# Kernel optimization log

Hardware: AMD Instinct MI355X
Metric: run time of the kernel (lower is better)

The kernel has to match this reference:

```python
import jax, jax.numpy as jnp
import numpy as np

N_NODES = 100000
N_EDGES = 6400000
MIN_DIST = 5.0


def setup_inputs() -> dict:
    key = jax.random.key(0)
    k1, k2, k3 = jax.random.split(key, 3)
    pos = jax.random.normal(k1, (N_NODES, 2), dtype=jnp.float32)
    vel = jax.random.normal(k2, (N_NODES, 2), dtype=jnp.float32)
    edge_index = jax.random.randint(k3, (2, N_EDGES), 0, N_NODES, dtype=jnp.int64)
    return {"pos": pos, "vel": vel, "edge_index": edge_index}


def reference(pos, vel, edge_index):
    # h = [pos, vel] per node, shape [N, 4]
    h = jnp.concatenate([pos, vel], axis=-1)
    src, dst = edge_index[0], edge_index[1]  # PyG: h_j = h[src], h_i = h[dst]
    h_dif = h[src] - h[dst]                  # [E, 4]
    pos_dif = h_dif[:, :2]                   # [E, 2]
    vel_dif = h_dif[:, 2:]                   # [E, 2]

    norm = jnp.linalg.norm(pos_dif, axis=1)  # [E]
    safe_norm = jnp.where(norm > 0, norm, 1.0)
    # coll = -sigmoid(-10*(|d|-min_dist)) * d/|d|, nan_to_num(0) where |d|==0
    coll = jnp.where(
        (norm > 0)[:, None],
        -jax.nn.sigmoid(-10.0 * (norm - MIN_DIST))[:, None] * pos_dif / safe_norm[:, None],
        0.0,
    )                                        # [E, 2]
    mean_in = pos_dif / 30.0 + vel_dif       # [E, 2]

    n = pos.shape[0]
    add_out = jax.ops.segment_sum(coll, dst, num_segments=n)      # scatter add
    sums = jax.ops.segment_sum(mean_in, dst, num_segments=n)
    counts = jax.ops.segment_sum(jnp.ones((dst.shape[0], 1), pos.dtype), dst, num_segments=n)
    mean_out = sums / jnp.maximum(counts, 1.0)                    # scatter mean

    return add_out * 5.0 + mean_out          # [N, 2] acceleration
```

## Files before the change

kernel.cpp:

```cpp
#include <hip/hip_runtime.h>


#define DC      200
#define NBK     512
#define NSEG    512
#define EPB     12500
#define ORDCAP  14400
#define KB      13
#define KMAX    15
#define BLOCK   256
#define BBLOCK  1024
#define FBLOCK  1024

__device__ __forceinline__ void edge_math(float4 hs, float4 hd,
                                          float& cx, float& cy, float& mx, float& my) {
    float px = hs.x - hd.x;
    float py = hs.y - hd.y;
    float vx = hs.z - hd.z;
    float vy = hs.w - hd.w;
    float norm = sqrtf(px * px + py * py);
    cx = 0.0f; cy = 0.0f;
    if (norm > 0.0f) {
        float sig = 1.0f / (1.0f + expf(10.0f * (norm - 5.0f)));
        float scale = -sig / norm;
        cx = scale * px;
        cy = scale * py;
    }
    mx = px * (1.0f / 30.0f) + vx;
    my = py * (1.0f / 30.0f) + vy;
}

__global__ void prep_kernel(const float2* __restrict__ pos2,
                            const float2* __restrict__ vel2,
                            float4* __restrict__ h4, int n) {
    int i = blockIdx.x * blockDim.x + threadIdx.x;
    if (i < n) {
        float2 p = pos2[i];
        float2 v = vel2[i];
        h4[i] = make_float4(p.x, p.y, v.x, v.y);
    }
}

__global__ __launch_bounds__(BBLOCK) void bin_kernel(
        const int* __restrict__ ei, unsigned* __restrict__ binsout,
        int* __restrict__ inclT, int n_edges, int nbb) {
    __shared__ int hist[NBK];
    __shared__ int cur[NBK];
    __shared__ unsigned ord[EPB];
    __shared__ int wsum[16];
    __shared__ int wbase[16];

    const int tid  = threadIdx.x;
    const int lane = tid & 63;
    const int wv   = tid >> 6;
    const int bx   = blockIdx.x;
    const long long e0 = (long long)bx * EPB;
    const int n_my = (int)min((long long)EPB, (long long)n_edges - e0);
    if (n_my <= 0) return;

    const int* __restrict__ srow = ei + e0;
    const int* __restrict__ drow = ei + n_edges + e0;

    for (int i = tid; i < NBK; i += BBLOCK) hist[i] = 0;
    __syncthreads();

    int      bq[KB];
    unsigned wq[KB];
    #pragma unroll
    for (int q = 0; q < KB; ++q) {
        int idx = tid + q * BBLOCK;
        if (idx < n_my) {
            int d = drow[idx];
            int s = srow[idx];
            int b = (unsigned)d / DC;
            bq[q] = b;
            wq[q] = ((unsigned)s << 8) | (unsigned)(d - b * DC);
            atomicAdd(&hist[b], 1);
        } else {
            bq[q] = -1;
        }
    }
    __syncthreads();

    const int nw = NBK >> 6;
    int myinc = 0, myh = 0, myi = 0;
    if (wv < nw) {
        myi = (wv << 6) + lane;
        myh = hist[myi];
        int v = myh;
        #pragma unroll
        for (int m = 1; m < 64; m <<= 1) {
            int u = __shfl_up(v, m);
            if (lane >= m) v += u;
        }
        myinc = v;
        if (lane == 63) wsum[wv] = v;
    }
    __syncthreads();
    if (tid == 0) {
        int run = 0;
        for (int w = 0; w < nw; ++w) { wbase[w] = run; run += wsum[w]; }
    }
    __syncthreads();
    if (wv < nw) {
        int inc = myinc + wbase[wv];
        cur[myi] = inc - myh;
        inclT[(size_t)myi * nbb + bx] = inc;
    }
    __syncthreads();

    #pragma unroll
    for (int q = 0; q < KB; ++q) {
        if (bq[q] >= 0) {
            int p = atomicAdd(&cur[bq[q]], 1);
            ord[p] = wq[q];
        }
    }
    __syncthreads();

    unsigned* __restrict__ bo = binsout + e0;
    for (int i = tid; i < n_my; i += BBLOCK) bo[i] = ord[i];
}

__global__ __launch_bounds__(FBLOCK) void fused_kernel(
        const float4* __restrict__ h4, const unsigned* __restrict__ binsout,
        const int* __restrict__ inclT, float* __restrict__ out,
        int nbb, int n_nodes) {
    __shared__ unsigned ord2[ORDCAP];
    __shared__ unsigned sstart[NSEG];
    __shared__ int spfx[NSEG + 1];
    __shared__ int hist[DC];
    __shared__ int pfx[DC + 1];
    __shared__ int cur[DC];
    __shared__ int wsum[16];
    __shared__ int wbase[16];

    const int tid  = threadIdx.x;
    const int lane = tid & 63;
    const int wv   = tid >> 6;
    const int dc   = blockIdx.x;

    for (int j = tid; j < nbb; j += FBLOCK) {
        int hi = inclT[(size_t)dc * nbb + j];
        int lo = (dc > 0) ? inclT[(size_t)(dc - 1) * nbb + j] : 0;
        sstart[j] = (unsigned)j * EPB + (unsigned)lo;
        spfx[j + 1] = hi - lo;
    }
    for (int i = tid; i < DC; i += FBLOCK) hist[i] = 0;
    if (tid == 0) spfx[0] = 0;
    __syncthreads();

    const int nw = (nbb + 63) >> 6;
    int myv = 0, myj = -1;
    if (wv < nw) {
        myj = (wv << 6) + lane;
        int v = (myj < nbb) ? spfx[myj + 1] : 0;
        #pragma unroll
        for (int m = 1; m < 64; m <<= 1) {
            int u = __shfl_up(v, m);
            if (lane >= m) v += u;
        }
        myv = v;
        if (lane == 63) wsum[wv] = v;
    }
    __syncthreads();
    if (tid == 0) {
        int run = 0;
        for (int w = 0; w < nw; ++w) { wbase[w] = run; run += wsum[w]; }
    }
    __syncthreads();
    if (wv < nw && myj < nbb) spfx[myj + 1] = myv + wbase[wv];
    __syncthreads();
    int tot = spfx[nbb];
    if (tot > ORDCAP) tot = ORDCAP;
    for (int j = nbb + tid; j < NSEG; j += FBLOCK) spfx[j + 1] = tot;
    __syncthreads();

    unsigned wq[KMAX];
    #pragma unroll
    for (int q = 0; q < KMAX; ++q) {
        int p = tid + q * FBLOCK;
        if (p < tot) {
            int lo = 0;
            #pragma unroll
            for (int st = NSEG / 2; st >= 1; st >>= 1)
                if (spfx[lo + st] <= p) lo += st;
            unsigned w = binsout[sstart[lo] + (unsigned)(p - spfx[lo])];
            wq[q] = w;
            atomicAdd(&hist[w & 255u], 1);
        }
    }
    __syncthreads();

    const int nwh = (DC + 63) >> 6;
    int mvr = 0, mr = -1, mh = 0;
    if (wv < nwh) {
        mr = (wv << 6) + lane;
        mh = (mr < DC) ? hist[mr] : 0;
        int v = mh;
        #pragma unroll
        for (int m = 1; m < 64; m <<= 1) {
            int u = __shfl_up(v, m);
            if (lane >= m) v += u;
        }
        mvr = v;
        if (lane == 63) wsum[8 + wv] = v;
    }
    __syncthreads();
    if (tid == 0) {
        int run = 0;
        for (int w = 0; w < nwh; ++w) { wbase[8 + w] = run; run += wsum[8 + w]; }
    }
    __syncthreads();
    if (wv < nwh && mr < DC) {
        int inc = mvr + wbase[8 + wv];
        pfx[mr + 1] = inc;
        cur[mr] = inc - mh;
        if (mr == 0) pfx[0] = 0;
    }
    __syncthreads();

    #pragma unroll
    for (int q = 0; q < KMAX; ++q) {
        int p = tid + q * FBLOCK;
        if (p < tot) {
            int pp = atomicAdd(&cur[wq[q] & 255u], 1);
            ord2[pp] = wq[q] >> 8;
        }
    }
    __syncthreads();

    const int grp = tid >> 4;
    const int gl  = tid & 15;
    const int base = dc * DC;
    for (int r = grp; r < DC; r += FBLOCK / 16) {
        int n = base + r;
        if (n < n_nodes) {
            int st = pfx[r], en = pfx[r + 1];
            int cnt = en - st;
            float4 hd = h4[n];
            float a0 = 0.f, a1 = 0.f, a2 = 0.f, a3 = 0.f;
            for (int k = st + gl; k < en; k += 16) {
                unsigned s = ord2[k];
                float4 hs = h4[s];
                float cx, cy, mx, my;
                edge_math(hs, hd, cx, cy, mx, my);
                a0 += cx; a1 += cy; a2 += mx; a3 += my;
            }
            #pragma unroll
            for (int m = 8; m >= 1; m >>= 1) {
                a0 += __shfl_xor(a0, m);
                a1 += __shfl_xor(a1, m);
                a2 += __shfl_xor(a2, m);
                a3 += __shfl_xor(a3, m);
            }
            if (gl == 0) {
                float inv = 1.0f / fmaxf((float)cnt, 1.0f);
                float2 o;
                o.x = a0 * 5.0f + a2 * inv;
                o.y = a1 * 5.0f + a3 * inv;
                reinterpret_cast<float2*>(out)[n] = o;
            }
        }
    }
}

__global__ void edge_kernel(const float* __restrict__ pos,
                            const float* __restrict__ vel,
                            const int* __restrict__ ei,
                            float* __restrict__ acc,
                            int n_nodes, int n_edges) {
    int e = blockIdx.x * blockDim.x + threadIdx.x;
    if (e >= n_edges) return;
    int s = ei[e];
    int d = ei[n_edges + e];
    const float2* pos2 = reinterpret_cast<const float2*>(pos);
    const float2* vel2 = reinterpret_cast<const float2*>(vel);
    float4 hs = make_float4(pos2[s].x, pos2[s].y, vel2[s].x, vel2[s].y);
    float4 hd = make_float4(pos2[d].x, pos2[d].y, vel2[d].x, vel2[d].y);
    float cx, cy, mx, my;
    edge_math(hs, hd, cx, cy, mx, my);
    atomicAdd(&acc[0 * n_nodes + d], cx);
    atomicAdd(&acc[1 * n_nodes + d], cy);
    atomicAdd(&acc[2 * n_nodes + d], mx);
    atomicAdd(&acc[3 * n_nodes + d], my);
    atomicAdd(&acc[4 * n_nodes + d], 1.0f);
}

__global__ void finalize_kernel(const float* __restrict__ acc,
                                float* __restrict__ out, int n_nodes) {
    int i = blockIdx.x * blockDim.x + threadIdx.x;
    if (i >= n_nodes) return;
    float cx = acc[0 * n_nodes + i];
    float cy = acc[1 * n_nodes + i];
    float mx = acc[2 * n_nodes + i];
    float my = acc[3 * n_nodes + i];
    float cnt = acc[4 * n_nodes + i];
    float inv = 1.0f / fmaxf(cnt, 1.0f);
    float2 o;
    o.x = cx * 5.0f + mx * inv;
    o.y = cy * 5.0f + my * inv;
    reinterpret_cast<float2*>(out)[i] = o;
}

extern "C" void kernel_launch(void* const* d_in, const int* in_sizes, int n_in,
                              void* d_out, int out_size, void* d_ws, size_t ws_size,
                              hipStream_t stream) {
    const float* pos = (const float*)d_in[0];
    const float* vel = (const float*)d_in[1];
    const int*   ei  = (const int*)d_in[2];
    float* out = (float*)d_out;

    int n_nodes = in_sizes[0] / 2;
    int n_edges = in_sizes[2] / 2;

    int ndc = (n_nodes + DC - 1) / DC;
    int nbb = (int)(((long long)n_edges + EPB - 1) / EPB);

    size_t h_off    = 0;
    size_t bo_off   = (h_off + (size_t)n_nodes * 16 + 511) & ~(size_t)511;
    size_t incl_off = (bo_off + (size_t)nbb * EPB * 4 + 511) & ~(size_t)511;
    size_t need     = incl_off + (size_t)NBK * nbb * 4;

    if (ndc <= NBK && nbb <= NSEG && need <= ws_size &&
        (unsigned)n_nodes < (1u << 24)) {
        float4*   h4      = (float4*)((char*)d_ws + h_off);
        unsigned* binsout = (unsigned*)((char*)d_ws + bo_off);
        int*      inclT   = (int*)((char*)d_ws + incl_off);

        int grid_p = (n_nodes + BLOCK - 1) / BLOCK;
        prep_kernel<<<grid_p, BLOCK, 0, stream>>>(
            (const float2*)pos, (const float2*)vel, h4, n_nodes);

        bin_kernel<<<nbb, BBLOCK, 0, stream>>>(ei, binsout, inclT,
                                               n_edges, nbb);

        fused_kernel<<<ndc, FBLOCK, 0, stream>>>(h4, binsout, inclT, out,
                                                 nbb, n_nodes);
    } else {
        float* acc = (float*)d_ws;
        hipMemsetAsync(d_ws, 0, (size_t)5 * n_nodes * sizeof(float), stream);
        int grid_e = (n_edges + BLOCK - 1) / BLOCK;
        edge_kernel<<<grid_e, BLOCK, 0, stream>>>(pos, vel, ei, acc, n_nodes, n_edges);
        int grid_n = (n_nodes + BLOCK - 1) / BLOCK;
        finalize_kernel<<<grid_n, BLOCK, 0, stream>>>(acc, out, n_nodes);
    }
}
```

Baseline: 145.0 us.

## Fuse node packing into bin kernel, vectorize edge IO, replace segment search with map

Removes the separate prep kernel by having each bin_kernel block pack a slice of pos/vel into the float4 node buffer, saving one launch. The bin kernel now loads edge indices and stores binned output as int4 vectors when the block is full and aligned, keeping a scalar fallback for other cases. In the fused kernel, the per-element binary search over segment prefixes is replaced by a ushort lookup map built in shared memory (aliased onto ord2) plus a per-segment offset. This adds a serial per-thread fill loop for the map and more registers for the 16-entry edge queues.

```diff
diff --git a/kernel.cpp b/kernel.cpp
--- a/kernel.cpp
+++ b/kernel.cpp
@@ -7,6 +7,7 @@
 #define EPB     12500
 #define ORDCAP  14400
 #define KB      13
+#define KBV     16
 #define KMAX    15
 #define BLOCK   256
 #define BBLOCK  1024
@@ -30,23 +31,15 @@
     my = py * (1.0f / 30.0f) + vy;
 }
 
-__global__ void prep_kernel(const float2* __restrict__ pos2,
-                            const float2* __restrict__ vel2,
-                            float4* __restrict__ h4, int n) {
-    int i = blockIdx.x * blockDim.x + threadIdx.x;
-    if (i < n) {
-        float2 p = pos2[i];
-        float2 v = vel2[i];
-        h4[i] = make_float4(p.x, p.y, v.x, v.y);
-    }
-}
-
 __global__ __launch_bounds__(BBLOCK) void bin_kernel(
-        const int* __restrict__ ei, unsigned* __restrict__ binsout,
-        int* __restrict__ inclT, int n_edges, int nbb) {
+        const int* __restrict__ ei,
+        const float2* __restrict__ pos2, const float2* __restrict__ vel2,
+        float4* __restrict__ h4, unsigned* __restrict__ binsout,
+        int* __restrict__ inclT, int n_edges, int nbb,
+        int n_nodes, int hpb) {
+    __shared__ __align__(16) unsigned ord[EPB];
     __shared__ int hist[NBK];
     __shared__ int cur[NBK];
-    __shared__ unsigned ord[EPB];
     __shared__ int wsum[16];
     __shared__ int wbase[16];
 
@@ -58,28 +51,65 @@
     const int n_my = (int)min((long long)EPB, (long long)n_edges - e0);
     if (n_my <= 0) return;
 
+    {
+        int i0 = bx * hpb;
+        int i1 = min(n_nodes, i0 + hpb);
+        for (int i = i0 + tid; i < i1; i += BBLOCK) {
+            float2 p = pos2[i];
+            float2 v = vel2[i];
+            h4[i] = make_float4(p.x, p.y, v.x, v.y);
+        }
+    }
+
     const int* __restrict__ srow = ei + e0;
     const int* __restrict__ drow = ei + n_edges + e0;
 
     for (int i = tid; i < NBK; i += BBLOCK) hist[i] = 0;
     __syncthreads();
 
-    int      bq[KB];
-    unsigned wq[KB];
-    #pragma unroll
-    for (int q = 0; q < KB; ++q) {
-        int idx = tid + q * BBLOCK;
-        if (idx < n_my) {
-            int d = drow[idx];
-            int s = srow[idx];
-            int b = (unsigned)d / DC;
-            bq[q] = b;
-            wq[q] = ((unsigned)s << 8) | (unsigned)(d - b * DC);
-            atomicAdd(&hist[b], 1);
-        } else {
-            bq[q] = -1;
-        }
-    }
+    const bool vec = (n_my == EPB) && ((n_edges & 3) == 0) && ((EPB & 3) == 0);
+    const int nvec = EPB >> 2;
+
+    int      bq[KBV];
+    unsigned wq[KBV];
+    #pragma unroll
+    for (int q = 0; q < KBV; ++q) bq[q] = -1;
+
+    if (vec) {
+        const int4* __restrict__ s4 = reinterpret_cast<const int4*>(srow);
+        const int4* __restrict__ d4 = reinterpret_cast<const int4*>(drow);
+        #pragma unroll
+        for (int q = 0; q < 4; ++q) {
+            int v = tid + q * BBLOCK;
+            if (v < nvec) {
+                int4 ss = s4[v];
+                int4 dd = d4[v];
+                #pragma unroll
+                for (int j = 0; j < 4; ++j) {
+                    int d = (&dd.x)[j];
+                    int s = (&ss.x)[j];
+                    int b = (int)((unsigned)d / DC);
+                    bq[q * 4 + j] = b;
+                    wq[q * 4 + j] = ((unsigned)s << 8) | (unsigned)(d - b * DC);
+                }
+            }
+        }
+    } else {
+        #pragma unroll
+        for (int q = 0; q < KB; ++q) {
+            int idx = tid + q * BBLOCK;
+            if (idx < n_my) {
+                int d = drow[idx];
+                int s = srow[idx];
+                int b = (int)((unsigned)d / DC);
+                bq[q] = b;
+                wq[q] = ((unsigned)s << 8) | (unsigned)(d - b * DC);
+            }
+        }
+    }
+    #pragma unroll
+    for (int q = 0; q < KBV; ++q)
+        if (bq[q] >= 0) atomicAdd(&hist[bq[q]], 1);
     __syncthreads();
 
     const int nw = NBK >> 6;
@@ -110,7 +140,7 @@
     __syncthreads();
 
     #pragma unroll
-    for (int q = 0; q < KB; ++q) {
+    for (int q = 0; q < KBV; ++q) {
         if (bq[q] >= 0) {
             int p = atomicAdd(&cur[bq[q]], 1);
             ord[p] = wq[q];
@@ -118,8 +148,14 @@
     }
     __syncthreads();
 
-    unsigned* __restrict__ bo = binsout + e0;
-    for (int i = tid; i < n_my; i += BBLOCK) bo[i] = ord[i];
+    if (vec) {
+        const int4* __restrict__ o4 = reinterpret_cast<const int4*>(ord);
+        int4* __restrict__ bo4 = reinterpret_cast<int4*>(binsout + e0);
+        for (int i = tid; i < nvec; i += BBLOCK) bo4[i] = o4[i];
+    } else {
+        unsigned* __restrict__ bo = binsout + e0;
+        for (int i = tid; i < n_my; i += BBLOCK) bo[i] = ord[i];
+    }
 }
 
 __global__ __launch_bounds__(FBLOCK) void fused_kernel(
@@ -127,14 +163,16 @@
         const int* __restrict__ inclT, float* __restrict__ out,
         int nbb, int n_nodes) {
     __shared__ unsigned ord2[ORDCAP];
-    __shared__ unsigned sstart[NSEG];
     __shared__ int spfx[NSEG + 1];
+    __shared__ int adj[NSEG];
     __shared__ int hist[DC];
     __shared__ int pfx[DC + 1];
     __shared__ int cur[DC];
     __shared__ int wsum[16];
     __shared__ int wbase[16];
 
+    unsigned short* map = reinterpret_cast<unsigned short*>(ord2);
+
     const int tid  = threadIdx.x;
     const int lane = tid & 63;
     const int wv   = tid >> 6;
@@ -143,7 +181,7 @@
     for (int j = tid; j < nbb; j += FBLOCK) {
         int hi = inclT[(size_t)dc * nbb + j];
         int lo = (dc > 0) ? inclT[(size_t)(dc - 1) * nbb + j] : 0;
-        sstart[j] = (unsigned)j * EPB + (unsigned)lo;
+        adj[j] = j * EPB + lo;
         spfx[j + 1] = hi - lo;
     }
     for (int i = tid; i < DC; i += FBLOCK) hist[i] = 0;
@@ -173,20 +211,22 @@
     __syncthreads();
     int tot = spfx[nbb];
     if (tot > ORDCAP) tot = ORDCAP;
-    for (int j = nbb + tid; j < NSEG; j += FBLOCK) spfx[j + 1] = tot;
-    __syncthreads();
-
-    unsigned wq[KMAX];
+    for (int j = tid; j < nbb; j += FBLOCK) {
+        int k0 = spfx[j];
+        int k1 = min(spfx[j + 1], ORDCAP);
+        adj[j] -= k0;
+        for (int k = k0; k < k1; ++k) map[k] = (unsigned short)j;
+    }
+    __syncthreads();
+
+    unsigned wqr[KMAX];
     #pragma unroll
     for (int q = 0; q < KMAX; ++q) {
         int p = tid + q * FBLOCK;
         if (p < tot) {
-            int lo = 0;
-            #pragma unroll
-            for (int st = NSEG / 2; st >= 1; st >>= 1)
-                if (spfx[lo + st] <= p) lo += st;
-            unsigned w = binsout[sstart[lo] + (unsigned)(p - spfx[lo])];
-            wq[q] = w;
+            int j = (int)map[p];
+            unsigned w = binsout[adj[j] + p];
+            wqr[q] = w;
             atomicAdd(&hist[w & 255u], 1);
         }
     }
@@ -224,8 +264,8 @@
     for (int q = 0; q < KMAX; ++q) {
         int p = tid + q * FBLOCK;
         if (p < tot) {
-            int pp = atomicAdd(&cur[wq[q] & 255u], 1);
-            ord2[pp] = wq[q] >> 8;
+            int pp = atomicAdd(&cur[wqr[q] & 255u], 1);
+            ord2[pp] = wqr[q] >> 8;
         }
     }
     __syncthreads();
@@ -316,6 +356,7 @@
 
     int ndc = (n_nodes + DC - 1) / DC;
     int nbb = (int)(((long long)n_edges + EPB - 1) / EPB);
+    int hpb = (n_nodes + nbb - 1) / nbb;
 
     size_t h_off    = 0;
     size_t bo_off   = (h_off + (size_t)n_nodes * 16 + 511) & ~(size_t)511;
@@ -328,12 +369,9 @@
         unsigned* binsout = (unsigned*)((char*)d_ws + bo_off);
         int*      inclT   = (int*)((char*)d_ws + incl_off);
 
-        int grid_p = (n_nodes + BLOCK - 1) / BLOCK;
-        prep_kernel<<<grid_p, BLOCK, 0, stream>>>(
-            (const float2*)pos, (const float2*)vel, h4, n_nodes);
-
-        bin_kernel<<<nbb, BBLOCK, 0, stream>>>(ei, binsout, inclT,
-                                               n_edges, nbb);
+        bin_kernel<<<nbb, BBLOCK, 0, stream>>>(
+            ei, (const float2*)pos, (const float2*)vel, h4,
+            binsout, inclT, n_edges, nbb, n_nodes, hpb);
 
         fused_kernel<<<ndc, FBLOCK, 0, stream>>>(h4, binsout, inclT, out,
                                                  nbb, n_nodes);
```

Result: faster. 139.8 us (-3.6%).
